# Kernel tuning notes

Measured on AMD Instinct MI355X. Metric: run time of the kernel, lower is better.

The kernel has to match this reference:

```python
import jax, jax.numpy as jnp
import numpy as np

SEQ_LEN = 4096
D_IN = 2048
D_OUT = 2048
DROPOUT_P = 0.5


def setup_inputs() -> dict:
    key = jax.random.key(0)
    kx, kq, kk, kv = jax.random.split(key, 4)
    return {
        "x": jax.random.normal(kx, (SEQ_LEN, D_IN), dtype=jnp.float32),
        "W_query": jax.random.uniform(kq, (D_IN, D_OUT), dtype=jnp.float32),
        "W_key": jax.random.uniform(kk, (D_IN, D_OUT), dtype=jnp.float32),
        "W_value": jax.random.uniform(kv, (D_IN, D_OUT), dtype=jnp.float32),
    }


def reference(x, W_query, W_key, W_value):
    # projections: [S, d_in] @ [d_in, d_out] -> [S, d_out]
    queries = x @ W_query
    keys = x @ W_key
    values = x @ W_value
    # full score matrix [S, S]
    attn_scores = queries @ keys.T
    S = attn_scores.shape[0]
    causal_mask = jnp.triu(jnp.ones((S, S), dtype=bool), k=1)
    masked = jnp.where(causal_mask, -jnp.inf, attn_scores)
    scale = jnp.sqrt(jnp.asarray(keys.shape[-1], dtype=masked.dtype))
    attn_weights = jax.nn.softmax(masked / scale, axis=1)
    # dropout p=0.5 (train mode), inverted scaling, deterministic key
    keep = jax.random.bernoulli(jax.random.key(42), 1.0 - DROPOUT_P, attn_weights.shape)
    attn_weights = jnp.where(keep, attn_weights / (1.0 - DROPOUT_P), 0.0)
    context_vec = attn_weights @ values  # [S, d_out]
    return context_vec
```

## Files before the change

### kernel.cpp

```cpp
#include <hip/hip_runtime.h>
#include <cstdint>
#include <cstddef>
#include <cmath>

#define SEQ 4096
#define DM  2048
#define NSC ((SEQ / 128) * (SEQ / 128 + 1) / 2)

typedef unsigned int u32;
typedef unsigned short u16;
typedef __attribute__((ext_vector_type(8))) short bf16x8;
typedef __attribute__((ext_vector_type(4))) float f32x4;
typedef __attribute__((ext_vector_type(16))) float f32x16;

__device__ __forceinline__ u16 f2bf(float f) {
  u32 u = __float_as_uint(f);
  return (u16)((u + 0x7FFFu + ((u >> 16) & 1u)) >> 16);
}
__device__ __forceinline__ float bf2f(u16 h) { return __uint_as_float(((u32)h) << 16); }

__device__ __forceinline__ u32 rotl32(u32 x, int r) { return (x << r) | (x >> (32 - r)); }

__device__ __forceinline__ void tf2x32(u32 c0, u32 c1, u32& o0, u32& o1) {
  const u32 k0 = 0u, k1 = 42u, k2 = 0x1BD11BDAu ^ 0u ^ 42u;
  u32 x0 = c0 + k0;
  u32 x1 = c1 + k1;
#define TFR(r) { x0 += x1; x1 = rotl32(x1, (r)); x1 ^= x0; }
  TFR(13) TFR(15) TFR(26) TFR(6)   x0 += k1; x1 += k2 + 1u;
  TFR(17) TFR(29) TFR(16) TFR(24)  x0 += k2; x1 += k0 + 2u;
  TFR(13) TFR(15) TFR(26) TFR(6)   x0 += k0; x1 += k1 + 3u;
  TFR(17) TFR(29) TFR(16) TFR(24)  x0 += k1; x1 += k2 + 4u;
  TFR(13) TFR(15) TFR(26) TFR(6)   x0 += k2; x1 += k0 + 5u;
#undef TFR
  o0 = x0; o1 = x1;
}

__device__ __forceinline__ bool dropout_keep(u32 idx) {
  u32 a, b; tf2x32(0u, idx, a, b);
  return (((a ^ b) & 0x80000000u) == 0u);
}

__device__ __forceinline__ void g2l16(const void* g, void* l) {
  __builtin_amdgcn_global_load_lds((const __attribute__((address_space(1))) u32*)g,
                                   (__attribute__((address_space(3))) u32*)l, 16, 0, 0);
}

#define MFMA16(a, b, c) __builtin_amdgcn_mfma_f32_16x16x32_bf16(a, b, c, 0, 0, 0)
#define MFMA32(a, b, c) __builtin_amdgcn_mfma_f32_32x32x16_bf16(a, b, c, 0, 0, 0)


__device__ __forceinline__ void gemm_core_split(
    const u16* __restrict__ Ah, const u16* __restrict__ AlFT,
    const u16* __restrict__ Bh, const u16* __restrict__ BlFT,
    int lda, int ldb, int rowBlock, int colBlock, int kmax,
    f32x16 (&acc)[2][2], u16* smem)
{
  u16* Als = smem;
  u16* Bls = smem + 8192;
  const int tid  = threadIdx.x;
  const int wid  = tid >> 6;
  const int lane = tid & 63;
  const int wr   = (wid & 1) << 6;
  const int wc   = (wid >> 1) << 6;
  const int l31  = lane & 31;
  const int lh   = lane >> 5;
  const int srow = wid * 32 + (lane >> 2);
  const int skol = (((lane & 3) ^ ((lane >> 3) & 3)) << 3);
  const int KA16 = lda >> 4, KB16 = ldb >> 4;
  const int rtA0 = (rowBlock >> 5) + ((wid & 1) << 1);
  const int rtB0 = (colBlock >> 5) + ((wid >> 1) << 1);
  const int swz  = (l31 >> 1) & 3;

  const f32x16 zero = {0.f,0.f,0.f,0.f,0.f,0.f,0.f,0.f,0.f,0.f,0.f,0.f,0.f,0.f,0.f,0.f};
#pragma unroll
  for (int i = 0; i < 2; ++i)
#pragma unroll
    for (int j = 0; j < 2; ++j) acc[i][j] = zero;

  for (int kb = 0; kb < kmax; kb += 64) {
#pragma unroll
    for (int h = 0; h < 2; ++h)
#pragma unroll
      for (int t = 0; t < 2; ++t) {
        const size_t ga = (size_t)(rowBlock + srow + t * 16) * lda + kb + h * 32 + skol;
        const size_t gb = (size_t)(colBlock + srow + t * 16) * ldb + kb + h * 32 + skol;
        const int lo = h * 4096 + (wid * 32 + t * 16) * 32;
        g2l16(Ah + ga, &Als[lo]);
        g2l16(Bh + gb, &Bls[lo]);
      }
    __syncthreads();

#pragma unroll
    for (int q = 0; q < 4; ++q) {
      const int h = q >> 1, s = q & 1;
      const int kt16 = (kb >> 4) + q;
      const int cl = s * 2 + lh;
      bf16x8 ah[2], bh[2], al[2], bl[2];
#pragma unroll
      for (int r = 0; r < 2; ++r) {
        const int rowA = wr + r * 32 + l31;
        const int rowB = wc + r * 32 + l31;
        ah[r] = *(const bf16x8*)&Als[h * 4096 + rowA * 32 + ((cl ^ swz) << 3)];
        bh[r] = *(const bf16x8*)&Bls[h * 4096 + rowB * 32 + ((cl ^ swz) << 3)];
        al[r] = *(const bf16x8*)(AlFT + (((size_t)(rtA0 + r) * KA16 + kt16) * 64 + lane) * 8);
        bl[r] = *(const bf16x8*)(BlFT + (((size_t)(rtB0 + r) * KB16 + kt16) * 64 + lane) * 8);
      }
#pragma unroll
      for (int r = 0; r < 2; ++r)
#pragma unroll
        for (int c = 0; c < 2; ++c) {
          acc[r][c] = MFMA32(ah[r], bh[c], acc[r][c]);
          acc[r][c] = MFMA32(ah[r], bl[c], acc[r][c]);
          acc[r][c] = MFMA32(al[r], bh[c], acc[r][c]);
        }
    }
    __syncthreads();
  }
}

__device__ __forceinline__ void gemm_core(
    const u16* __restrict__ Ah, const u16* __restrict__ Bh,
    int lda, int ldb, int rowBlock, int colBlock, int kmax,
    f32x4 (&acc)[4][4], u16* smem)
{
  u16* Als = smem;
  u16* Bls = smem + 8192;
  const int tid  = threadIdx.x;
  const int wid  = tid >> 6;
  const int lane = tid & 63;
  const int wr   = (wid & 1) << 6;
  const int wc   = (wid >> 1) << 6;
  const int lrow = lane & 15;
  const int lk   = (((lane >> 4) ^ ((lrow >> 1) & 3)) << 3);
  const int srow = wid * 32 + (lane >> 2);
  const int skol = (((lane & 3) ^ ((lane >> 3) & 3)) << 3);

  const f32x4 zero = {0.f, 0.f, 0.f, 0.f};
#pragma unroll
  for (int i = 0; i < 4; ++i)
#pragma unroll
    for (int j = 0; j < 4; ++j) acc[i][j] = zero;

  for (int kb = 0; kb < kmax; kb += 64) {
#pragma unroll
    for (int h = 0; h < 2; ++h)
#pragma unroll
      for (int t = 0; t < 2; ++t) {
        const size_t ga = (size_t)(rowBlock + srow + t * 16) * lda + kb + h * 32 + skol;
        const size_t gb = (size_t)(colBlock + srow + t * 16) * ldb + kb + h * 32 + skol;
        const int lo = h * 4096 + (wid * 32 + t * 16) * 32;
        g2l16(Ah + ga, &Als[lo]);
        g2l16(Bh + gb, &Bls[lo]);
      }
    __syncthreads();

#pragma unroll
    for (int h = 0; h < 2; ++h) {
      bf16x8 ah[4], bh[4];
#pragma unroll
      for (int r = 0; r < 4; ++r) {
        ah[r] = *(const bf16x8*)&Als[h * 4096 + (wr + r * 16 + lrow) * 32 + lk];
        bh[r] = *(const bf16x8*)&Bls[h * 4096 + (wc + r * 16 + lrow) * 32 + lk];
      }
#pragma unroll
      for (int r = 0; r < 4; ++r)
#pragma unroll
        for (int c = 0; c < 4; ++c)
          acc[r][c] = MFMA16(ah[r], bh[c], acc[r][c]);
    }
    __syncthreads();
  }
}

__global__ __launch_bounds__(256) void k_split_all(
    const float* __restrict__ X, u16* __restrict__ Xh, u16* __restrict__ Xl,
    const float* __restrict__ Wq, const float* __restrict__ Wk, const float* __restrict__ Wv,
    u16* __restrict__ Wqh, u16* __restrict__ Wql,
    u16* __restrict__ Wkh, u16* __restrict__ Wkl, u16* __restrict__ Wvh) {
  __shared__ float t[64][65];
  const int bid = blockIdx.x;
  const int tid = threadIdx.x;
  const int wid = tid >> 6, lane = tid & 63;

  if (bid < 4096) {
    const int kt16 = bid & 127;
    const int rt32 = (bid >> 7) * 4 + wid;
    const int row = rt32 * 32 + (lane & 31);
    const int col = kt16 * 16 + ((lane >> 5) << 3);
    const float* src = X + (size_t)row * DM + col;
    const float4 v0 = *(const float4*)src;
    const float4 v1 = *(const float4*)(src + 4);
    float v[8] = {v0.x, v0.y, v0.z, v0.w, v1.x, v1.y, v1.z, v1.w};
    u16 h[8], l[8];
#pragma unroll
    for (int j = 0; j < 8; ++j) {
      h[j] = f2bf(v[j]);
      l[j] = f2bf(v[j] - bf2f(h[j]));
    }
    u16* hp = Xh + (size_t)row * DM + col;
    *(ushort4*)hp = *(ushort4*)&h[0];
    *(ushort4*)(hp + 4) = *(ushort4*)&h[4];
    u16* lp = Xl + (((size_t)rt32 * 128 + kt16) * 64 + lane) * 8;
    *(ushort4*)lp = *(ushort4*)&l[0];
    *(ushort4*)(lp + 4) = *(ushort4*)&l[4];
    return;
  }

  const int r = bid - 4096;
  const int z = r >> 10;
  const int rem = r & 1023;
  const int n0 = (rem & 31) * 64, k0 = (rem >> 5) * 64;
  const float* W = (z == 0) ? Wq : (z == 1) ? Wk : Wv;
  u16* Oh = (z == 0) ? Wqh : (z == 1) ? Wkh : Wvh;
  u16* Ol = (z == 0) ? Wql : Wkl;
  const int tx = tid & 63, ty = tid >> 6;
#pragma unroll
  for (int i = 0; i < 16; ++i)
    t[ty * 16 + i][tx] = W[(size_t)(k0 + ty * 16 + i) * DM + n0 + tx];
  __syncthreads();
  {
    const int nl = tid >> 2, kc = (tid & 3) * 16;
    u16 h[16];
#pragma unroll
    for (int i = 0; i < 16; ++i) h[i] = f2bf(t[kc + i][nl]);
    u16* hp = Oh + (size_t)(n0 + nl) * DM + k0 + kc;
#pragma unroll
    for (int i = 0; i < 4; ++i) *(ushort4*)(hp + i * 4) = *(ushort4*)&h[i * 4];
  }
  if (z < 2) {
#pragma unroll
    for (int tt = 0; tt < 2; ++tt) {
      const int idx = wid * 2 + tt;
      const int rt = idx >> 2, kt = idx & 3;
      const int nl = rt * 32 + (lane & 31);
      const int kc = kt * 16 + ((lane >> 5) << 3);
      u16 l[8];
#pragma unroll
      for (int j = 0; j < 8; ++j) {
        const float v = t[kc + j][nl];
        l[j] = f2bf(v - bf2f(f2bf(v)));
      }
      const int rtg = (n0 >> 5) + rt, ktg = (k0 >> 4) + kt;
      u16* lp = Ol + (((size_t)rtg * (DM / 16) + ktg) * 64 + lane) * 8;
      *(ushort4*)lp = *(ushort4*)&l[0];
      *(ushort4*)(lp + 4) = *(ushort4*)&l[4];
    }
  }
}

__global__ __launch_bounds__(256) void k_proj_qkv(
    const u16* __restrict__ Xh, const u16* __restrict__ Xl,
    const u16* __restrict__ Wqh, const u16* __restrict__ Wql,
    const u16* __restrict__ Wkh, const u16* __restrict__ Wkl,
    const u16* __restrict__ Wvh,
    u16* __restrict__ Qh, u16* __restrict__ Ql,
    u16* __restrict__ Kh, u16* __restrict__ Kl,
    u16* __restrict__ Vt, float rscaleQ)
{
  __shared__ __align__(16) u16 smem[16384];
  const int z = blockIdx.z;
  const int rowBlock = blockIdx.y * 128, colBlock = blockIdx.x * 128;
  const int lane = threadIdx.x & 63, wid = threadIdx.x >> 6;

  if (z == 2) {
    f32x4 acc[4][4];
    gemm_core(Xh, Wvh, DM, DM, rowBlock, colBlock, DM, acc, smem);
    const int r0 = rowBlock + ((wid & 1) << 6) + ((lane >> 4) << 2);
    const int c0 = colBlock + ((wid >> 1) << 6) + (lane & 15);
#pragma unroll
    for (int r = 0; r < 4; ++r)
#pragma unroll
      for (int c = 0; c < 4; ++c) {
        ushort4 pk;
        pk.x = f2bf(acc[r][c][0]); pk.y = f2bf(acc[r][c][1]);
        pk.z = f2bf(acc[r][c][2]); pk.w = f2bf(acc[r][c][3]);
        *(ushort4*)(Vt + (size_t)(c0 + c * 16) * SEQ + r0 + r * 16) = pk;
      }
    return;
  }

  const u16* Bh = z ? Wkh : Wqh;
  const u16* Bl = z ? Wkl : Wql;
  u16* Oh = z ? Kh : Qh;
  u16* Ol = z ? Kl : Ql;
  const float rs = z ? 1.0f : rscaleQ;
  f32x16 acc[2][2];
  gemm_core_split(Xh, Xl, Bh, Bl, DM, DM, rowBlock, colBlock, DM, acc, smem);

  const int wr = (wid & 1) << 6, wc = (wid >> 1) << 6;
  const int l31 = lane & 31, lh = lane >> 5;
#pragma unroll
  for (int r = 0; r < 2; ++r)
#pragma unroll
    for (int c = 0; c < 2; ++c) {
      const int colL = wc + c * 32 + l31;
      const int colG = colBlock + colL;
#pragma unroll
      for (int g = 0; g < 4; ++g)
#pragma unroll
        for (int e = 0; e < 4; ++e) {
          const int rowL = wr + r * 32 + 4 * lh + e + 8 * g;
          const float v = acc[r][c][g * 4 + e] * rs;
          const u16 h = f2bf(v);
          Oh[(size_t)(rowBlock + rowL) * DM + colG] = h;
          smem[rowL * 128 + (((colL >> 3) ^ (rowL & 7)) << 3) + (colL & 7)] =
              f2bf(v - bf2f(h));
        }
    }
  __syncthreads();
#pragma unroll
  for (int t8 = 0; t8 < 8; ++t8) {
    const int idx = wid * 8 + t8;
    const int rt = idx >> 3, kt = idx & 7;
    const int rowL = rt * 32 + l31;
    const int ch = kt * 2 + lh;
    const bf16x8 vL = *(const bf16x8*)&smem[rowL * 128 + ((ch ^ (rowL & 7)) << 3)];
    const int rtg = (rowBlock >> 5) + rt, ktg = (colBlock >> 4) + kt;
    *(bf16x8*)(Ol + (((size_t)rtg * (DM / 16) + ktg) * 64 + lane) * 8) = vL;
  }
}

__global__ __launch_bounds__(256) void k_scores(
    const u16* __restrict__ Qh, const u16* __restrict__ Ql,
    const u16* __restrict__ Kh, const u16* __restrict__ Kl, float* __restrict__ S)
{
  __shared__ __align__(16) u16 smem[16384];
  const int bid = blockIdx.x;
  int by = (int)((sqrtf(8.0f * (float)bid + 1.0f) - 1.0f) * 0.5f);
  while ((by + 1) * (by + 2) / 2 <= bid) ++by;
  while (by * (by + 1) / 2 > bid) --by;
  const int bx = bid - by * (by + 1) / 2;

  f32x16 acc[2][2];
  gemm_core_split(Qh, Ql, Kh, Kl, DM, DM, by * 128, bx * 128, DM, acc, smem);

  const int lane = threadIdx.x & 63, wid = threadIdx.x >> 6;
  const int wr = (wid & 1) << 6, wc = (wid >> 1) << 6;
  const int l31 = lane & 31, lh = lane >> 5;
  const int r0 = by * 128 + wr, c0 = bx * 128 + wc;
#pragma unroll
  for (int r = 0; r < 2; ++r)
#pragma unroll
    for (int c = 0; c < 2; ++c) {
      const int col = c0 + c * 32 + l31;
#pragma unroll
      for (int g = 0; g < 4; ++g)
#pragma unroll
        for (int e = 0; e < 4; ++e) {
          const int row = r0 + r * 32 + 4 * lh + e + 8 * g;
          S[(size_t)row * SEQ + col] = acc[r][c][g * 4 + e];
        }
    }
}

__global__ __launch_bounds__(256) void k_softmax_dropout(const float* __restrict__ S,
                                                         u16* __restrict__ P) {
  const int row = blockIdx.x;
  const int n = row + 1;
  const int nt = (n + 1023) >> 10;
  const int tid = threadIdx.x;
  __shared__ float buf[SEQ];
  __shared__ float red[4];
  __shared__ float bcast;
  const float* srow = S + (size_t)row * SEQ;

  float lmax = -INFINITY;
  for (int t = 0; t < nt; ++t) {
    int j4 = tid + t * 256;
    float4 v = *(const float4*)(srow + (size_t)j4 * 4);
    int b = j4 * 4;
    float x0 = (b + 0 < n) ? v.x : -INFINITY;
    float x1 = (b + 1 < n) ? v.y : -INFINITY;
    float x2 = (b + 2 < n) ? v.z : -INFINITY;
    float x3 = (b + 3 < n) ? v.w : -INFINITY;
    buf[b + 0] = x0; buf[b + 1] = x1; buf[b + 2] = x2; buf[b + 3] = x3;
    lmax = fmaxf(lmax, fmaxf(fmaxf(x0, x1), fmaxf(x2, x3)));
  }
  for (int off = 32; off > 0; off >>= 1) lmax = fmaxf(lmax, __shfl_down(lmax, off, 64));
  if ((tid & 63) == 0) red[tid >> 6] = lmax;
  __syncthreads();
  if (tid == 0) bcast = fmaxf(fmaxf(red[0], red[1]), fmaxf(red[2], red[3]));
  __syncthreads();
  const float m = bcast;

  float lsum = 0.f;
  for (int t = 0; t < nt; ++t) {
    int b = (tid + t * 256) * 4;
    float e0 = expf(buf[b + 0] - m);
    float e1 = expf(buf[b + 1] - m);
    float e2 = expf(buf[b + 2] - m);
    float e3 = expf(buf[b + 3] - m);
    buf[b + 0] = e0; buf[b + 1] = e1; buf[b + 2] = e2; buf[b + 3] = e3;
    lsum += (e0 + e1) + (e2 + e3);
  }
  for (int off = 32; off > 0; off >>= 1) lsum += __shfl_down(lsum, off, 64);
  if ((tid & 63) == 0) red[tid >> 6] = lsum;
  __syncthreads();
  if (tid == 0) bcast = (red[0] + red[1]) + (red[2] + red[3]);
  __syncthreads();
  const float total = bcast;

  u16* prow = P + (size_t)row * SEQ;
  const int zeroEnd = ((row >> 7) + 1) << 7;
  for (int j = tid; j < zeroEnd; j += 256) {
    float out = 0.f;
    if (j < n) {
      const float w = buf[j] / total;
      out = dropout_keep((u32)(row * SEQ + j)) ? w * 2.0f : 0.f;
    }
    prow[j] = f2bf(out);
  }
}

__global__ __launch_bounds__(256) void k_pv(const u16* __restrict__ P,
                                            const u16* __restrict__ Vt,
                                            float* __restrict__ O) {
  __shared__ __align__(16) u16 smem[16384];
  const int by = (SEQ / 128 - 1) - blockIdx.y;
  f32x4 acc[4][4];
  gemm_core(P, Vt, SEQ, SEQ, by * 128, blockIdx.x * 128, (by + 1) * 128, acc, smem);

  const int lane = threadIdx.x & 63, wid = threadIdx.x >> 6;
  const int r0 = by * 128 + ((wid & 1) << 6) + ((lane >> 4) << 2);
  const int c0 = blockIdx.x * 128 + ((wid >> 1) << 6) + (lane & 15);
#pragma unroll
  for (int r = 0; r < 4; ++r)
#pragma unroll
    for (int c = 0; c < 4; ++c)
#pragma unroll
      for (int e = 0; e < 4; ++e)
        O[(size_t)(r0 + r * 16 + e) * DM + (c0 + c * 16)] = acc[r][c][e];
}

extern "C" void kernel_launch(void* const* d_in, const int* in_sizes, int n_in,
                              void* d_out, int out_size, void* d_ws, size_t ws_size,
                              hipStream_t stream) {
  const float* x  = (const float*)d_in[0];
  const float* Wq = (const float*)d_in[1];
  const float* Wk = (const float*)d_in[2];
  const float* Wv = (const float*)d_in[3];

  const size_t PL = (size_t)SEQ * DM;
  const size_t WL = (size_t)DM * DM;
  u16* base = (u16*)d_ws;
  u16* Qh = base;
  u16* Ql = Qh + PL;
  u16* Kh = Ql + PL;
  u16* Kl = Kh + PL;
  u16* Vt = Kl + PL;
  u16* P  = base;
  u16* regA = Vt + PL;
  u16* Xh  = regA;
  u16* Xl  = Xh + PL;
  u16* Wqh = Xl + PL;
  u16* Wql = Wqh + WL;
  u16* Wkh = Wql + WL;
  u16* Wkl = Wkh + WL;
  u16* Wvh = Wkl + WL;
  float* S = (float*)regA;

  const float rscale = 1.0f / sqrtf(2048.0f);
  dim3 blk(256);
  k_split_all<<<dim3(4096 + 3 * 1024), blk, 0, stream>>>(x, Xh, Xl, Wq, Wk, Wv,
                                                         Wqh, Wql, Wkh, Wkl, Wvh);
  k_proj_qkv<<<dim3(DM / 128, SEQ / 128, 3), blk, 0, stream>>>(
      Xh, Xl, Wqh, Wql, Wkh, Wkl, Wvh, Qh, Ql, Kh, Kl, Vt, rscale);
  k_scores<<<dim3(NSC), blk, 0, stream>>>(Qh, Ql, Kh, Kl, S);
  k_softmax_dropout<<<dim3(SEQ), blk, 0, stream>>>(S, P);
  k_pv<<<dim3(DM / 128, SEQ / 128), blk, 0, stream>>>(P, Vt, (float*)d_out);
}
```

Before: 657.4 us.

## Split QKV projection into larger-tile pipelined Q/K and V GEMM kernels

Replaces the combined 128x128 QKV projection kernel with two kernels. The first is a 256x256-tile, 512-thread Q/K split-bf16 GEMM that double-buffers LDS with direct global-to-LDS loads and reads the low-part operands straight from global memory in fragment layout. The second is a separate 256x128-tile V GEMM with the same pipelining. Larger tiles raise data reuse per block and the explicit prefetch and priority scheduling aim to hide memory latency. In exchange the kernels use much more LDS and more registers, and there is one extra kernel launch.

```diff
diff --git a/kernel.cpp b/kernel.cpp
--- a/kernel.cpp
+++ b/kernel.cpp
@@ -248,76 +248,220 @@
   }
 }
 
-__global__ __launch_bounds__(256) void k_proj_qkv(
+__global__ __launch_bounds__(512, 2) void k_proj_qk(
     const u16* __restrict__ Xh, const u16* __restrict__ Xl,
     const u16* __restrict__ Wqh, const u16* __restrict__ Wql,
     const u16* __restrict__ Wkh, const u16* __restrict__ Wkl,
-    const u16* __restrict__ Wvh,
     u16* __restrict__ Qh, u16* __restrict__ Ql,
-    u16* __restrict__ Kh, u16* __restrict__ Kl,
-    u16* __restrict__ Vt, float rscaleQ)
+    u16* __restrict__ Kh, u16* __restrict__ Kl, float rscaleQ)
 {
-  __shared__ __align__(16) u16 smem[16384];
+  __shared__ __align__(16) u16 smem[65536];
   const int z = blockIdx.z;
-  const int rowBlock = blockIdx.y * 128, colBlock = blockIdx.x * 128;
-  const int lane = threadIdx.x & 63, wid = threadIdx.x >> 6;
-
-  if (z == 2) {
-    f32x4 acc[4][4];
-    gemm_core(Xh, Wvh, DM, DM, rowBlock, colBlock, DM, acc, smem);
-    const int r0 = rowBlock + ((wid & 1) << 6) + ((lane >> 4) << 2);
-    const int c0 = colBlock + ((wid >> 1) << 6) + (lane & 15);
+  const u16* __restrict__ Bw = z ? Wkh : Wqh;
+  const u16* __restrict__ Bl = z ? Wkl : Wql;
+  u16* __restrict__ Oh = z ? Kh : Qh;
+  u16* __restrict__ Ol = z ? Kl : Ql;
+  const float rs = z ? 1.0f : rscaleQ;
+
+  const int rowBlock = blockIdx.y * 256;
+  const int colBlock = blockIdx.x * 256;
+  const int tid  = threadIdx.x;
+  const int wid  = tid >> 6, lane = tid & 63;
+  const int wm   = wid >> 2, wn = wid & 3;
+  const int l31  = lane & 31, lh = lane >> 5;
+  const int srow = tid >> 2, schunk = tid & 3;
+  const int sko  = ((schunk ^ ((srow >> 1) & 3)) << 3);
+  const int rkey = (l31 >> 1) & 3;
+  const int rtA0 = (rowBlock >> 5) + wm * 4;
+  const int rtB0 = (colBlock >> 5) + wn * 2;
+
+  f32x16 acc[4][2];
+  {
+    const f32x16 z16 = {0.f,0.f,0.f,0.f,0.f,0.f,0.f,0.f,0.f,0.f,0.f,0.f,0.f,0.f,0.f,0.f};
 #pragma unroll
     for (int r = 0; r < 4; ++r)
 #pragma unroll
-      for (int c = 0; c < 4; ++c) {
-        ushort4 pk;
-        pk.x = f2bf(acc[r][c][0]); pk.y = f2bf(acc[r][c][1]);
-        pk.z = f2bf(acc[r][c][2]); pk.w = f2bf(acc[r][c][3]);
-        *(ushort4*)(Vt + (size_t)(c0 + c * 16) * SEQ + r0 + r * 16) = pk;
-      }
-    return;
-  }
-
-  const u16* Bh = z ? Wkh : Wqh;
-  const u16* Bl = z ? Wkl : Wql;
-  u16* Oh = z ? Kh : Qh;
-  u16* Ol = z ? Kl : Ql;
-  const float rs = z ? 1.0f : rscaleQ;
-  f32x16 acc[2][2];
-  gemm_core_split(Xh, Xl, Bh, Bl, DM, DM, rowBlock, colBlock, DM, acc, smem);
-
-  const int wr = (wid & 1) << 6, wc = (wid >> 1) << 6;
-  const int l31 = lane & 31, lh = lane >> 5;
-#pragma unroll
-  for (int r = 0; r < 2; ++r)
+      for (int c = 0; c < 2; ++c) acc[r][c] = z16;
+  }
+  bf16x8 alo0[4], blo0[2], alo1[4], blo1[2];
+
+#define QK_STG(hh, pp) { \
+    g2l16(Xh + (size_t)(rowBlock + (pp)*128 + srow) * DM + kbn + (hh)*32 + sko, \
+          &smem[bufN + (hh)*8192 + (pp)*4096 + tid*8]); \
+    g2l16(Bw + (size_t)(colBlock + (pp)*128 + srow) * DM + kbn + (hh)*32 + sko, \
+          &smem[bufN + 16384 + (hh)*8192 + (pp)*4096 + tid*8]); }
+
+#define QK_LO(AV, BV, kt) { \
+    const int kk_ = (kt); \
+    _Pragma("unroll") for (int r_ = 0; r_ < 4; ++r_) \
+      AV[r_] = *(const bf16x8*)(Xl + (((size_t)(rtA0 + r_) * 128 + kk_) * 64 + lane) * 8); \
+    _Pragma("unroll") for (int c_ = 0; c_ < 2; ++c_) \
+      BV[c_] = *(const bf16x8*)(Bl + (((size_t)(rtB0 + c_) * 128 + kk_) * 64 + lane) * 8); }
+
+#define QK_PH(qq, ALC, BLC, ALN, BLN, STMT, ktn) { \
+    __builtin_amdgcn_sched_barrier(0); \
+    QK_LO(ALN, BLN, ktn); \
+    __builtin_amdgcn_sched_barrier(0); \
+    STMT; \
+    bf16x8 ah[4], bh[2]; \
+    const int cl_ = ((qq) & 1) * 2 + lh; \
+    const int hx_ = (qq) >> 1; \
+    _Pragma("unroll") for (int r_ = 0; r_ < 4; ++r_) \
+      ah[r_] = *(const bf16x8*)&smem[bufC + ((hx_*256 + wm*128 + r_*32 + l31) << 5) + ((cl_ ^ rkey) << 3)]; \
+    _Pragma("unroll") for (int c_ = 0; c_ < 2; ++c_) \
+      bh[c_] = *(const bf16x8*)&smem[bufC + 16384 + ((hx_*256 + wn*64 + c_*32 + l31) << 5) + ((cl_ ^ rkey) << 3)]; \
+    __builtin_amdgcn_s_setprio(1); \
+    _Pragma("unroll") for (int r_ = 0; r_ < 4; ++r_) \
+      _Pragma("unroll") for (int c_ = 0; c_ < 2; ++c_) { \
+        acc[r_][c_] = MFMA32(ah[r_], bh[c_], acc[r_][c_]); \
+        acc[r_][c_] = MFMA32(ah[r_], BLC[c_], acc[r_][c_]); \
+        acc[r_][c_] = MFMA32(ALC[r_], bh[c_], acc[r_][c_]); } \
+    __builtin_amdgcn_s_setprio(0); }
+
+  {
+    const size_t kbn = 0; const int bufN = 0;
+    QK_STG(0,0) QK_STG(0,1) QK_STG(1,0) QK_STG(1,1)
+  }
+  QK_LO(alo0, blo0, 0);
+  asm volatile("s_waitcnt vmcnt(0)" ::: "memory");
+  __builtin_amdgcn_s_barrier();
+
+  for (int t = 0; t < 32; ++t) {
+    const int bufC = (t & 1) << 15;
+    const int bufN = bufC ^ 32768;
+    const size_t kbn = (size_t)(t + 1) * 64;
+    const bool more = (t < 31);
+    const int g4 = t * 4;
+    QK_PH(0, alo0, blo0, alo1, blo1, if (more) { QK_STG(0,0) QK_STG(0,1) }, g4 + 1)
+    QK_PH(1, alo1, blo1, alo0, blo0, if (more) { QK_STG(1,0) QK_STG(1,1) }, g4 + 2)
+    QK_PH(2, alo0, blo0, alo1, blo1, ;, g4 + 3)
+    QK_PH(3, alo1, blo1, alo0, blo0, ;, (g4 + 4 < 128 ? g4 + 4 : 127))
+    asm volatile("s_waitcnt vmcnt(0)" ::: "memory");
+    __builtin_amdgcn_s_barrier();
+  }
+#undef QK_PH
+#undef QK_LO
+#undef QK_STG
+
+  __syncthreads();
+  u16* scr = smem + wid * 8192;
+  const int r0g = rowBlock + wm * 128;
+  const int c0g = colBlock + wn * 64;
+#pragma unroll
+  for (int r = 0; r < 4; ++r)
 #pragma unroll
     for (int c = 0; c < 2; ++c) {
-      const int colL = wc + c * 32 + l31;
-      const int colG = colBlock + colL;
+      const int colL = c * 32 + l31;
 #pragma unroll
       for (int g = 0; g < 4; ++g)
 #pragma unroll
         for (int e = 0; e < 4; ++e) {
-          const int rowL = wr + r * 32 + 4 * lh + e + 8 * g;
+          const int rowL = r * 32 + 8 * g + 4 * lh + e;
           const float v = acc[r][c][g * 4 + e] * rs;
           const u16 h = f2bf(v);
-          Oh[(size_t)(rowBlock + rowL) * DM + colG] = h;
-          smem[rowL * 128 + (((colL >> 3) ^ (rowL & 7)) << 3) + (colL & 7)] =
+          Oh[(size_t)(r0g + rowL) * DM + c0g + colL] = h;
+          scr[rowL * 64 + (((colL >> 3) ^ (rowL & 7)) << 3) + (colL & 7)] =
               f2bf(v - bf2f(h));
         }
     }
-  __syncthreads();
-#pragma unroll
-  for (int t8 = 0; t8 < 8; ++t8) {
-    const int idx = wid * 8 + t8;
-    const int rt = idx >> 3, kt = idx & 7;
-    const int rowL = rt * 32 + l31;
-    const int ch = kt * 2 + lh;
-    const bf16x8 vL = *(const bf16x8*)&smem[rowL * 128 + ((ch ^ (rowL & 7)) << 3)];
-    const int rtg = (rowBlock >> 5) + rt, ktg = (colBlock >> 4) + kt;
-    *(bf16x8*)(Ol + (((size_t)rtg * (DM / 16) + ktg) * 64 + lane) * 8) = vL;
-  }
+  asm volatile("s_waitcnt lgkmcnt(0)" ::: "memory");
+  __builtin_amdgcn_sched_barrier(0);
+#pragma unroll
+  for (int rt = 0; rt < 4; ++rt)
+#pragma unroll
+    for (int kt = 0; kt < 4; ++kt) {
+      const int rowL = rt * 32 + l31;
+      const int cl2 = kt * 2 + lh;
+      const bf16x8 v = *(const bf16x8*)&scr[rowL * 64 + ((cl2 ^ (rowL & 7)) << 3)];
+      const int rtg = (rowBlock >> 5) + wm * 4 + rt;
+      const int ktg = (colBlock >> 4) + wn * 4 + kt;
+      *(bf16x8*)(Ol + (((size_t)rtg * 128 + ktg) * 64 + lane) * 8) = v;
+    }
+}
+
+__global__ __launch_bounds__(512, 2) void k_proj_v(
+    const u16* __restrict__ Xh, const u16* __restrict__ Wvh, u16* __restrict__ Vt)
+{
+  __shared__ __align__(16) u16 smem[49152];
+  const int rowBlock = blockIdx.y * 256;
+  const int colBlock = blockIdx.x * 128;
+  const int tid  = threadIdx.x;
+  const int wid  = tid >> 6, lane = tid & 63;
+  const int wm   = wid >> 1, wn = wid & 1;
+  const int l31  = lane & 31, lh = lane >> 5;
+  const int srow = tid >> 2, schunk = tid & 3;
+  const int sko  = ((schunk ^ ((srow >> 1) & 3)) << 3);
+  const int rkey = (l31 >> 1) & 3;
+
+  f32x16 acc[2][2];
+  {
+    const f32x16 z16 = {0.f,0.f,0.f,0.f,0.f,0.f,0.f,0.f,0.f,0.f,0.f,0.f,0.f,0.f,0.f,0.f};
+#pragma unroll
+    for (int r = 0; r < 2; ++r)
+#pragma unroll
+      for (int c = 0; c < 2; ++c) acc[r][c] = z16;
+  }
+
+#define V_STGA(hh, pp) g2l16(Xh + (size_t)(rowBlock + (pp)*128 + srow) * DM + kbn + (hh)*32 + sko, \
+                             &smem[bufN + (hh)*8192 + (pp)*4096 + tid*8]);
+#define V_STGB(hh)     g2l16(Wvh + (size_t)(colBlock + srow) * DM + kbn + (hh)*32 + sko, \
+                             &smem[bufN + 16384 + (hh)*4096 + tid*8]);
+
+#define V_PH(qq, STMT) { \
+    __builtin_amdgcn_sched_barrier(0); \
+    STMT; \
+    bf16x8 ah[2], bh[2]; \
+    const int cl_ = ((qq) & 1) * 2 + lh; \
+    const int hx_ = (qq) >> 1; \
+    _Pragma("unroll") for (int r_ = 0; r_ < 2; ++r_) \
+      ah[r_] = *(const bf16x8*)&smem[bufC + ((hx_*256 + wm*64 + r_*32 + l31) << 5) + ((cl_ ^ rkey) << 3)]; \
+    _Pragma("unroll") for (int c_ = 0; c_ < 2; ++c_) \
+      bh[c_] = *(const bf16x8*)&smem[bufC + 16384 + ((hx_*128 + wn*64 + c_*32 + l31) << 5) + ((cl_ ^ rkey) << 3)]; \
+    __builtin_amdgcn_s_setprio(1); \
+    _Pragma("unroll") for (int r_ = 0; r_ < 2; ++r_) \
+      _Pragma("unroll") for (int c_ = 0; c_ < 2; ++c_) \
+        acc[r_][c_] = MFMA32(ah[r_], bh[c_], acc[r_][c_]); \
+    __builtin_amdgcn_s_setprio(0); }
+
+  {
+    const size_t kbn = 0; const int bufN = 0;
+    V_STGA(0,0) V_STGA(0,1) V_STGA(1,0) V_STGA(1,1) V_STGB(0) V_STGB(1)
+  }
+  asm volatile("s_waitcnt vmcnt(0)" ::: "memory");
+  __builtin_amdgcn_s_barrier();
+
+  for (int t = 0; t < 32; ++t) {
+    const int bufC = (t & 1) * 24576;
+    const int bufN = bufC ^ 24576;
+    const size_t kbn = (size_t)(t + 1) * 64;
+    const bool more = (t < 31);
+    V_PH(0, if (more) { V_STGA(0,0) V_STGA(0,1) V_STGB(0) })
+    V_PH(1, if (more) { V_STGA(1,0) V_STGA(1,1) V_STGB(1) })
+    V_PH(2, ;)
+    V_PH(3, ;)
+    asm volatile("s_waitcnt vmcnt(0)" ::: "memory");
+    __builtin_amdgcn_s_barrier();
+  }
+#undef V_PH
+#undef V_STGB
+#undef V_STGA
+
+  const int vr0 = rowBlock + wm * 64;
+#pragma unroll
+  for (int r = 0; r < 2; ++r)
+#pragma unroll
+    for (int c = 0; c < 2; ++c) {
+      const int col = colBlock + wn * 64 + c * 32 + l31;
+#pragma unroll
+      for (int g = 0; g < 4; ++g) {
+        ushort4 pk;
+        pk.x = f2bf(acc[r][c][g * 4 + 0]);
+        pk.y = f2bf(acc[r][c][g * 4 + 1]);
+        pk.z = f2bf(acc[r][c][g * 4 + 2]);
+        pk.w = f2bf(acc[r][c][g * 4 + 3]);
+        *(ushort4*)(Vt + (size_t)col * SEQ + vr0 + r * 32 + 8 * g + 4 * lh) = pk;
+      }
+    }
 }
 
 __global__ __launch_bounds__(256) void k_scores(
@@ -460,12 +604,12 @@
   float* S = (float*)regA;
 
   const float rscale = 1.0f / sqrtf(2048.0f);
-  dim3 blk(256);
-  k_split_all<<<dim3(4096 + 3 * 1024), blk, 0, stream>>>(x, Xh, Xl, Wq, Wk, Wv,
-                                                         Wqh, Wql, Wkh, Wkl, Wvh);
-  k_proj_qkv<<<dim3(DM / 128, SEQ / 128, 3), blk, 0, stream>>>(
-      Xh, Xl, Wqh, Wql, Wkh, Wkl, Wvh, Qh, Ql, Kh, Kl, Vt, rscale);
-  k_scores<<<dim3(NSC), blk, 0, stream>>>(Qh, Ql, Kh, Kl, S);
-  k_softmax_dropout<<<dim3(SEQ), blk, 0, stream>>>(S, P);
-  k_pv<<<dim3(DM / 128, SEQ / 128), blk, 0, stream>>>(P, Vt, (float*)d_out);
-}
+  k_split_all<<<dim3(4096 + 3 * 1024), dim3(256), 0, stream>>>(
+      x, Xh, Xl, Wq, Wk, Wv, Wqh, Wql, Wkh, Wkl, Wvh);
+  k_proj_qk<<<dim3(DM / 256, SEQ / 256, 2), dim3(512), 0, stream>>>(
+      Xh, Xl, Wqh, Wql, Wkh, Wkl, Qh, Ql, Kh, Kl, rscale);
+  k_proj_v<<<dim3(DM / 128, SEQ / 256), dim3(512), 0, stream>>>(Xh, Wvh, Vt);
+  k_scores<<<dim3(NSC), dim3(256), 0, stream>>>(Qh, Ql, Kh, Kl, S);
+  k_softmax_dropout<<<dim3(SEQ), dim3(256), 0, stream>>>(S, P);
+  k_pv<<<dim3(DM / 128, SEQ / 128), dim3(256), 0, stream>>>(P, Vt, (float*)d_out);
+}
```

After: 614.7 us. -6.5%, faster.
